# Performance work log

Hardware: AMD Instinct MI355X
Metric: run time of the kernel (lower is better)

The kernel has to match this reference:

```python
import jax, jax.numpy as jnp
import numpy as np

MAX_DISP = 4  # matches init_kwargs


def setup_inputs() -> dict:
    key = jax.random.key(0)
    k1, k2 = jax.random.split(key)
    x_1 = jax.random.normal(k1, (8, 64, 256, 256), dtype=jnp.float32)
    x_2 = jax.random.normal(k2, (8, 64, 256, 256), dtype=jnp.float32)
    return {"x_1": x_1, "x_2": x_2}


def reference(x_1, x_2):
    md = MAX_DISP
    B, C, H, W = x_1.shape
    # zero-pad x_2 spatially by max_disp on all sides
    x2p = jnp.pad(x_2, ((0, 0), (0, 0), (md, md), (md, md)))
    D = 2 * md + 1
    # row-major over (dx, dy), matching torch.meshgrid(indexing='ij')
    outs = [
        jnp.mean(x_1 * jax.lax.dynamic_slice(x2p, (0, 0, dx, dy), (B, C, H, W)),
                 axis=1, keepdims=True)
        for dx in range(D) for dy in range(D)
    ]
    return jnp.concatenate(outs, axis=1)  # [B, D*D, H, W]
```

## Files before the change

kernel.cpp:

```cpp
#include <hip/hip_runtime.h>


namespace {
constexpr int kB = 8;
constexpr int kC = 64;
constexpr int kH = 256;
constexpr int kW = 256;
constexpr int kD = 9;
constexpr int kMD = 4;
constexpr int kChanStride = kH * kW;
}

__global__ __launch_bounds__(64) void corr_kernel(
    const float* __restrict__ x1, const float* __restrict__ x2,
    float* __restrict__ out) {
  const int xcd  = blockIdx.x & 7;
  const int slot = blockIdx.x >> 3;
  const int b  = xcd;
  const int hp = slot / kD;
  const int dx = slot - hp * kD;

  const int lane = (int)threadIdx.x;
  const int half = lane >> 5;
  const int lh   = lane & 31;
  const int h    = hp * 2 + half;
  const int row  = h + dx - kMD;
  const int w0   = lh * 8;

  const bool rowok = (row >= 0) && (row < kH);
  const bool hasL  = rowok && (lh > 0);
  const bool hasR  = rowok && (lh < 31);

  float acc[kD][8];
#pragma unroll
  for (int dy = 0; dy < kD; ++dy)
#pragma unroll
    for (int j = 0; j < 8; ++j) acc[dy][j] = 0.0f;

  const float* p1 = x1 + ((size_t)(b * kC) * kH + h) * kW + w0;
  const float* p2 = x2 + ((size_t)(b * kC) * kH + row) * kW + w0;

  const float4 z = make_float4(0.f, 0.f, 0.f, 0.f);

  float4 a0, a1, t0, t1, t2, t3;
  a0 = *reinterpret_cast<const float4*>(p1);
  a1 = *reinterpret_cast<const float4*>(p1 + 4);
  t0 = hasL  ? *reinterpret_cast<const float4*>(p2 - 4) : z;
  t1 = rowok ? *reinterpret_cast<const float4*>(p2)     : z;
  t2 = rowok ? *reinterpret_cast<const float4*>(p2 + 4) : z;
  t3 = hasR  ? *reinterpret_cast<const float4*>(p2 + 8) : z;

#pragma unroll 2
  for (int c = 0; c < kC - 1; ++c) {
    p1 += kChanStride;
    p2 += kChanStride;
    float4 na0 = *reinterpret_cast<const float4*>(p1);
    float4 na1 = *reinterpret_cast<const float4*>(p1 + 4);
    float4 nt0 = hasL  ? *reinterpret_cast<const float4*>(p2 - 4) : z;
    float4 nt1 = rowok ? *reinterpret_cast<const float4*>(p2)     : z;
    float4 nt2 = rowok ? *reinterpret_cast<const float4*>(p2 + 4) : z;
    float4 nt3 = hasR  ? *reinterpret_cast<const float4*>(p2 + 8) : z;

    {
      const float av[8] = {a0.x, a0.y, a0.z, a0.w, a1.x, a1.y, a1.z, a1.w};
      const float t[16] = {t0.x, t0.y, t0.z, t0.w, t1.x, t1.y, t1.z, t1.w,
                           t2.x, t2.y, t2.z, t2.w, t3.x, t3.y, t3.z, t3.w};
#pragma unroll
      for (int dy = 0; dy < kD; ++dy)
#pragma unroll
        for (int j = 0; j < 8; ++j)
          acc[dy][j] = fmaf(av[j], t[dy + j], acc[dy][j]);
    }

    a0 = na0; a1 = na1; t0 = nt0; t1 = nt1; t2 = nt2; t3 = nt3;
  }
  {
    const float av[8] = {a0.x, a0.y, a0.z, a0.w, a1.x, a1.y, a1.z, a1.w};
    const float t[16] = {t0.x, t0.y, t0.z, t0.w, t1.x, t1.y, t1.z, t1.w,
                         t2.x, t2.y, t2.z, t2.w, t3.x, t3.y, t3.z, t3.w};
#pragma unroll
    for (int dy = 0; dy < kD; ++dy)
#pragma unroll
      for (int j = 0; j < 8; ++j)
        acc[dy][j] = fmaf(av[j], t[dy + j], acc[dy][j]);
  }

  const float inv = 1.0f / (float)kC;
  float* po = out + (((size_t)b * (kD * kD) + dx * kD) * kH + h) * kW + w0;
#pragma unroll
  for (int dy = 0; dy < kD; ++dy) {
    float4 o0 = make_float4(acc[dy][0] * inv, acc[dy][1] * inv,
                            acc[dy][2] * inv, acc[dy][3] * inv);
    float4 o1 = make_float4(acc[dy][4] * inv, acc[dy][5] * inv,
                            acc[dy][6] * inv, acc[dy][7] * inv);
    *reinterpret_cast<float4*>(po)     = o0;
    *reinterpret_cast<float4*>(po + 4) = o1;
    po += (size_t)kH * kW;
  }
}

extern "C" void kernel_launch(void* const* d_in, const int* in_sizes, int n_in,
                              void* d_out, int out_size, void* d_ws, size_t ws_size,
                              hipStream_t stream) {
  const float* x1 = (const float*)d_in[0];
  const float* x2 = (const float*)d_in[1];
  float* out = (float*)d_out;
  const int grid = kB * (kH / 2) * kD;
  corr_kernel<<<grid, 64, 0, stream>>>(x1, x2, out);
}
```

Baseline: 232.9 us.

## Merge nine dx blocks into one 576-thread block with periodic barriers

Measured after the change: 245.2 us. 5.3% more time.

```diff
diff --git a/kernel.cpp b/kernel.cpp
--- a/kernel.cpp
+++ b/kernel.cpp
@@ -8,23 +8,21 @@
 constexpr int kW = 256;
 constexpr int kD = 9;
 constexpr int kMD = 4;
-constexpr int kChanStride = kH * kW;
+constexpr int kCS = kH * kW;
 }
 
-__global__ __launch_bounds__(64) void corr_kernel(
+__global__ __launch_bounds__(576) void corr_kernel(
     const float* __restrict__ x1, const float* __restrict__ x2,
     float* __restrict__ out) {
-  const int xcd  = blockIdx.x & 7;
-  const int slot = blockIdx.x >> 3;
-  const int b  = xcd;
-  const int hp = slot / kD;
-  const int dx = slot - hp * kD;
-
-  const int lane = (int)threadIdx.x;
+  const int bb = blockIdx.x & 7;
+  const int hp = blockIdx.x >> 3;
+  const int tid  = (int)threadIdx.x;
+  const int wv   = tid >> 6;
+  const int lane = tid & 63;
   const int half = lane >> 5;
   const int lh   = lane & 31;
-  const int h    = hp * 2 + half;
-  const int row  = h + dx - kMD;
+  const int h    = 2 * hp + half;
+  const int row  = h + wv - kMD;
   const int w0   = lh * 8;
 
   const bool rowok = (row >= 0) && (row < kH);
@@ -37,9 +35,8 @@
 #pragma unroll
     for (int j = 0; j < 8; ++j) acc[dy][j] = 0.0f;
 
-  const float* p1 = x1 + ((size_t)(b * kC) * kH + h) * kW + w0;
-  const float* p2 = x2 + ((size_t)(b * kC) * kH + row) * kW + w0;
-
+  const float* p1 = x1 + ((size_t)(bb * kC) * kH + h) * kW + w0;
+  const float* p2 = x2 + ((size_t)(bb * kC) * kH + row) * kW + w0;
   const float4 z = make_float4(0.f, 0.f, 0.f, 0.f);
 
   float4 a0, a1, t0, t1, t2, t3;
@@ -52,8 +49,8 @@
 
 #pragma unroll 2
   for (int c = 0; c < kC - 1; ++c) {
-    p1 += kChanStride;
-    p2 += kChanStride;
+    p1 += kCS;
+    p2 += kCS;
     float4 na0 = *reinterpret_cast<const float4*>(p1);
     float4 na1 = *reinterpret_cast<const float4*>(p1 + 4);
     float4 nt0 = hasL  ? *reinterpret_cast<const float4*>(p2 - 4) : z;
@@ -73,6 +70,8 @@
     }
 
     a0 = na0; a1 = na1; t0 = nt0; t1 = nt1; t2 = nt2; t3 = nt3;
+
+    if ((c & 7) == 6) __syncthreads();
   }
   {
     const float av[8] = {a0.x, a0.y, a0.z, a0.w, a1.x, a1.y, a1.z, a1.w};
@@ -86,13 +85,13 @@
   }
 
   const float inv = 1.0f / (float)kC;
-  float* po = out + (((size_t)b * (kD * kD) + dx * kD) * kH + h) * kW + w0;
+  float* po = out + (((size_t)bb * (kD * kD) + wv * kD) * kH + h) * kW + w0;
 #pragma unroll
   for (int dy = 0; dy < kD; ++dy) {
-    float4 o0 = make_float4(acc[dy][0] * inv, acc[dy][1] * inv,
-                            acc[dy][2] * inv, acc[dy][3] * inv);
-    float4 o1 = make_float4(acc[dy][4] * inv, acc[dy][5] * inv,
-                            acc[dy][6] * inv, acc[dy][7] * inv);
+    const float4 o0 = make_float4(acc[dy][0] * inv, acc[dy][1] * inv,
+                                  acc[dy][2] * inv, acc[dy][3] * inv);
+    const float4 o1 = make_float4(acc[dy][4] * inv, acc[dy][5] * inv,
+                                  acc[dy][6] * inv, acc[dy][7] * inv);
     *reinterpret_cast<float4*>(po)     = o0;
     *reinterpret_cast<float4*>(po + 4) = o1;
     po += (size_t)kH * kW;
@@ -105,6 +104,6 @@
   const float* x1 = (const float*)d_in[0];
   const float* x2 = (const float*)d_in[1];
   float* out = (float*)d_out;
-  const int grid = kB * (kH / 2) * kD;
-  corr_kernel<<<grid, 64, 0, stream>>>(x1, x2, out);
+  const int grid = kB * (kH / 2);
+  corr_kernel<<<grid, 576, 0, stream>>>(x1, x2, out);
 }
```
